# Performance work log

Measured on AMD Instinct MI355X. Metric: run time of the kernel, lower is better.

The kernel has to match this reference:

```python
import jax, jax.numpy as jnp
import numpy as np
from jax import lax

EPS = 1e-9
DN = ('NCHW', 'OIHW', 'NCHW')


def _conv2d_valid(x, w):
    return lax.conv_general_dilated(x, w, window_strides=(1, 1), padding='VALID',
                                    dimension_numbers=DN)


def setup_inputs() -> dict:
    key = jax.random.key(0)
    kx, ky = jax.random.split(key)
    x = jax.random.normal(kx, (32, 64, 96, 96), dtype=jnp.float32)
    y = jax.random.normal(ky, (32, 64, 13, 13), dtype=jnp.float32)  # (K prototypes, C, kh, kw)
    return {'x': x, 'y': y}


def reference(x, y):
    # Per-prototype L2 normalization of y over (C, kh, kw)
    y_norm = jnp.clip(jnp.sqrt(jnp.sum(y * y, axis=(1, 2, 3), keepdims=True)), EPS)
    normed_y = y / y_norm
    # Sliding-window L2 norm of x. The torch code convolves x^2 with ones of
    # shape (K, C, kh, kw) producing K identical channels; we compute one
    # channel and broadcast (same math, less work).
    ones_k = jnp.ones((1,) + y.shape[1:], dtype=x.dtype)
    x_norm = jnp.clip(jnp.sqrt(_conv2d_valid(x * x, ones_k)), EPS)  # (B,1,H',W')
    diss = _conv2d_valid(x, normed_y) / x_norm  # (B,K,H',W')
    return jax.nn.relu(diss)
```

## Files before the change

kernel.cpp:

```cpp
#include <hip/hip_runtime.h>
#include <hip/hip_bf16.h>

#define B_   32
#define C_   64
#define H_   96
#define W_   96
#define K_   32
#define R_   13
#define HO_  84
#define WO_  84
#define HW_  (H_*W_)
#define OHW_ (HO_*WO_)
#define CRR_ (C_*R_*R_)
#define RR_  (R_*R_)

#define TILE_ 16
#define PW_   28
#define TLV_  24
#define PH_   36
#define NPIX2_ (PH_*PW_)
#define NEL2_  (2*NPIX2_)
#define HB2_   (NPIX2_*16)
#define BUF2_  (2*HB2_)
#define NPIX_ (PW_*PW_)
#define REGB_ (NPIX_*16)
#define LDS_FB (2*REGB_)

#define XBF_BYTES  ((size_t)B_*4*HW_*32)
#define UG_BYTES   ((size_t)RR_*4096)
#define S_BYTES    ((size_t)B_*HW_*4)
#define INV_BYTES  ((size_t)B_*OHW_*4)
#define WS_NEED    (XBF_BYTES + UG_BYTES + S_BYTES + INV_BYTES)

typedef unsigned int u32;
typedef unsigned short u16;
typedef __attribute__((ext_vector_type(16))) float f32x16;
typedef __attribute__((ext_vector_type(4))) u32 u32x4;

static __device__ __forceinline__ u16 f2bf(float v){
    __hip_bfloat16 h = __float2bfloat16(v);
    return *reinterpret_cast<u16*>(&h);
}

#define MFMA(acc, a, b) asm("v_mfma_f32_32x32x16_bf16 %0, %1, %2, %0" \
                            : "+v"(acc) : "v"(a), "v"(b))

static __device__ __forceinline__ void gload_lds16(const void* g, void* l){
    __builtin_amdgcn_global_load_lds(
        (const __attribute__((address_space(1))) unsigned char*)g,
        (__attribute__((address_space(3))) unsigned char*)l, 16, 0, 0);
}

static __device__ void prep_y_block(const float* __restrict__ y,
                                    unsigned char* __restrict__ u_g,
                                    int k, int tid, float* red){
    const float* yk = y + (size_t)k * CRR_;
    float ss = 0.f;
    for (int idx = tid; idx < CRR_; idx += 256){ float v = yk[idx]; ss += v*v; }
    for (int off = 32; off; off >>= 1) ss += __shfl_down(ss, off);
    if ((tid & 63) == 0) red[tid >> 6] = ss;
    __syncthreads();
    float inv = 1.f / fmaxf(sqrtf(red[0]+red[1]+red[2]+red[3]), 1e-9f);

    int c = tid & 63, grp = tid >> 6;
    int inoff = (k << 5) | ((c & 15) << 1);
    for (int base = 0; base < RR_; base += 4){
        int ij = base + grp;
        if (ij < RR_){
            int i = ij / R_, jx = ij % R_;
            float v = yk[c*RR_ + ij] * inv;
            size_t slice = ((size_t)(c >> 4) * RR_ + jx*R_ + i) << 10;
            *(u16*)(u_g + slice + inoff) = f2bf(v);
        }
    }
}

__global__ void k_prep_y(const float* __restrict__ y, unsigned char* __restrict__ u_g){
    __shared__ float red[4];
    prep_y_block(y, u_g, blockIdx.x, threadIdx.x, red);
}

__global__ void k_prep(const float* __restrict__ x, const float* __restrict__ y,
                       float* __restrict__ s, unsigned char* __restrict__ xbf,
                       unsigned char* __restrict__ u_g){
    __shared__ float red[4];
    int bb = blockIdx.x;
    if (bb < K_){ prep_y_block(y, u_g, bb, threadIdx.x, red); return; }
    int idx = (bb - K_)*256 + threadIdx.x;
    int b = idx / HW_, r = idx % HW_;
    const float* xb = x + (size_t)b * C_ * HW_ + r;
    float acc = 0.f;
    #pragma unroll
    for (int q = 0; q < 4; ++q){
        int c0 = q*16;
        float a0 = xb[(size_t)(c0+0)*HW_],  a1 = xb[(size_t)(c0+1)*HW_];
        float a2 = xb[(size_t)(c0+2)*HW_],  a3 = xb[(size_t)(c0+3)*HW_];
        float a4 = xb[(size_t)(c0+4)*HW_],  a5 = xb[(size_t)(c0+5)*HW_];
        float a6 = xb[(size_t)(c0+6)*HW_],  a7 = xb[(size_t)(c0+7)*HW_];
        float a8 = xb[(size_t)(c0+8)*HW_],  a9 = xb[(size_t)(c0+9)*HW_];
        float aa = xb[(size_t)(c0+10)*HW_], ab = xb[(size_t)(c0+11)*HW_];
        float ac = xb[(size_t)(c0+12)*HW_], ad = xb[(size_t)(c0+13)*HW_];
        float ae = xb[(size_t)(c0+14)*HW_], af = xb[(size_t)(c0+15)*HW_];
        acc += a0*a0+a1*a1+a2*a2+a3*a3+a4*a4+a5*a5+a6*a6+a7*a7
             + a8*a8+a9*a9+aa*aa+ab*ab+ac*ac+ad*ad+ae*ae+af*af;
        u32x4 q0 = { f2bf(a0)|((u32)f2bf(a1)<<16), f2bf(a2)|((u32)f2bf(a3)<<16),
                     f2bf(a4)|((u32)f2bf(a5)<<16), f2bf(a6)|((u32)f2bf(a7)<<16) };
        u32x4 q1 = { f2bf(a8)|((u32)f2bf(a9)<<16), f2bf(aa)|((u32)f2bf(ab)<<16),
                     f2bf(ac)|((u32)f2bf(ad)<<16), f2bf(ae)|((u32)f2bf(af)<<16) };
        unsigned char* ob = xbf + ((size_t)(b*4 + q)*HW_ + r)*32;
        *(u32x4*)(ob)      = q0;
        *(u32x4*)(ob + 16) = q1;
    }
    s[idx] = acc;
}

__global__ void k_sq(const float* __restrict__ x, float* __restrict__ s){
    int idx = blockIdx.x*256 + threadIdx.x;
    int b = idx / HW_, r = idx % HW_;
    const float* xb = x + (size_t)b * C_ * HW_;
    float acc = 0.f;
    #pragma unroll
    for (int c = 0; c < C_; ++c){ float v = xb[(size_t)c*HW_ + r]; acc += v*v; }
    s[idx] = acc;
}

__global__ void k_inv(const float* __restrict__ s, float* __restrict__ inv_xn){
    int idx = blockIdx.x*256 + threadIdx.x;
    int b = idx / OHW_, r = idx % OHW_;
    int oh = r / WO_, ow = r % WO_;
    const float* sb = s + (size_t)b*HW_ + oh*W_ + ow;
    float acc = 0.f;
    for (int i = 0; i < R_; ++i){
        #pragma unroll
        for (int j = 0; j < R_; ++j) acc += sb[i*W_ + j];
    }
    inv_xn[idx] = 1.f / fmaxf(sqrtf(acc), 1e-9f);
}

__launch_bounds__(256, 3)
__global__ void k_main(const unsigned char* __restrict__ xbf,
                       const unsigned char* __restrict__ u_g,
                       const float* __restrict__ inv_xn, float* __restrict__ out){
    extern __shared__ unsigned char lds[];

    int bb0 = blockIdx.x;
    int bb  = (bb0 & 7) * 96 + (bb0 >> 3);
    int b  = bb / 24;
    int tt = bb % 24;
    int oy = (tt / 6) * TLV_;
    int ox = (tt % 6) * TILE_;

    int tid  = threadIdx.x;
    int lane = tid & 63;
    int wv   = tid >> 6;
    int ks   = lane >> 5;
    int rb   = (lane >> 4) & 1;
    int cx   = lane & 15;
    int kpr  = lane & 31;

    const unsigned char* xq = xbf + (size_t)b*4*HW_*32;
    int aoff = (kpr << 5) + (ks << 4);
    int pb   = (6*wv + rb) * PW_ + cx;

    int goff[8], loff[8];
    #pragma unroll
    for (int j = 0; j < 8; ++j){
        int cb = wv + 4*j;
        int cs = cb*64; if (cs > NEL2_-64) cs = NEL2_-64;
        int e = cs + lane;
        int h = (e >= NPIX2_);
        int p = e - (h ? NPIX2_ : 0);
        int py = p / PW_, px = p % PW_;
        int gy = oy + py; if (gy > H_-1) gy = H_-1;
        int gx = ox + px; if (gx > W_-1) gx = W_-1;
        goff[j] = ((gy*W_ + gx) << 5) + h*16;
        loff[j] = cs << 4;
    }

#define STAGE(q) {                                                           \
        const unsigned char* src = xq + (size_t)(q)*HW_*32;                  \
        _Pragma("unroll")                                                    \
        for (int j = 0; j < 8; ++j)                                          \
            gload_lds16(src + goff[j], lds + loff[j]);                       \
    }

    f32x16 acc0 = {}, acc1 = {}, acc2 = {};
    STAGE(0);
    __syncthreads();

    for (int pass = 0; pass < 4; ++pass){
        const unsigned char* xh = lds + ks*HB2_;
        const unsigned char* ug = u_g + ((size_t)pass*RR_ << 10);

        u32x4 A0 = *(const u32x4*)(ug              + aoff);
        u32x4 A1 = *(const u32x4*)(ug + (1 << 10)  + aoff);
        u32x4 A2 = *(const u32x4*)(ug + (2 << 10)  + aoff);
        u32x4 A3 = *(const u32x4*)(ug + (3 << 10)  + aoff);

        const unsigned char* col0 = xh + pb*16;
        u32x4 w0 = *(const u32x4*)(col0);
        u32x4 w1 = *(const u32x4*)(col0 +   PW_*16);
        u32x4 w2 = *(const u32x4*)(col0 + 2*PW_*16);
        u32x4 w3 = *(const u32x4*)(col0 + 3*PW_*16);
        u32x4 w4 = *(const u32x4*)(col0 + 4*PW_*16);
        u32x4 w5 = *(const u32x4*)(col0 + 5*PW_*16);

        int t = 0;
        for (int jx = 0; jx < R_; ++jx){
            const unsigned char* col  = xh + (pb + jx)*16;
            const unsigned char* ncol = col + 16;
            u32x4 e0, e1, e2, e3, e4, e5;
            #pragma unroll
            for (int i = 0; i < R_; ++i, ++t){
                int tn = t + 4; if (tn > RR_-1) tn = RR_-1;
                u32x4 An = *(const u32x4*)(ug + ((size_t)tn << 10) + aoff);
                u32x4 wn = w5;
                if (i < 11) wn = *(const u32x4*)(col + (i+6)*PW_*16);
                if (i == 7)  e0 = *(const u32x4*)(ncol);
                if (i == 8)  e1 = *(const u32x4*)(ncol +   PW_*16);
                if (i == 9)  e2 = *(const u32x4*)(ncol + 2*PW_*16);
                if (i == 10) e3 = *(const u32x4*)(ncol + 3*PW_*16);
                if (i == 11) e4 = *(const u32x4*)(ncol + 4*PW_*16);
                if (i == 12) e5 = *(const u32x4*)(ncol + 5*PW_*16);
                __builtin_amdgcn_s_setprio(1);
                MFMA(acc0, A0, w0);
                MFMA(acc1, A0, w2);
                MFMA(acc2, A0, w4);
                __builtin_amdgcn_s_setprio(0);
                A0 = A1; A1 = A2; A2 = A3; A3 = An;
                w0 = w1; w1 = w2; w2 = w3; w3 = w4; w4 = w5; w5 = wn;
            }
            w0 = e0; w1 = e1; w2 = e2; w3 = e3; w4 = e4; w5 = e5;
        }

        if (pass < 3){
            __syncthreads();
            STAGE(pass+1);
            __syncthreads();
        }
    }

    int ow = ox + cx;
#define EPI(ACC, F) {                                                        \
        int oh = oy + 6*wv + rb + 2*(F);                                     \
        bool valid = (oh < HO_) && (ow < WO_);                               \
        float inv = 0.f;                                                     \
        if (valid) inv = inv_xn[(size_t)b*OHW_ + oh*WO_ + ow];               \
        float* ob = out + (size_t)b*K_*OHW_ + oh*WO_ + ow;                   \
        _Pragma("unroll")                                                    \
        for (int r = 0; r < 16; ++r){                                        \
            int kp = (r & 3) + 8*(r >> 2) + 4*ks;                            \
            if (valid) ob[(size_t)kp*OHW_] = fmaxf(ACC[r], 0.f) * inv;       \
        }                                                                    \
    }
    EPI(acc0, 0); EPI(acc1, 1); EPI(acc2, 2);
#undef EPI
}

__launch_bounds__(256, 4)
__global__ void k_main_fb(const float* __restrict__ x, const unsigned char* __restrict__ u_g,
                          const float* __restrict__ inv_xn, float* __restrict__ out){
    extern __shared__ unsigned char lds[];
    int bb = blockIdx.x;
    int b  = bb / 36;
    int tt = bb % 36;
    int oy = (tt / 6) * TILE_;
    int ox = (tt % 6) * TILE_;
    int tid  = threadIdx.x;
    int lane = tid & 63;
    int wv   = tid >> 6;
    int ks   = lane >> 5;
    int rb   = (lane >> 4) & 1;
    int cx   = lane & 15;
    int kpr  = lane & 31;
    const float* xb = x + (size_t)b * C_ * HW_;
    int aoff = (kpr << 5) + (ks << 4);
    int pb   = (4*wv + rb) * PW_ + cx;
    f32x16 acc0 = {}, acc1 = {};
    for (int pass = 0; pass < 4; ++pass){
        if (pass) __syncthreads();
        int cbase = pass << 4;
        for (int p = tid; p < NPIX_; p += 256){
            int py = p / PW_, px = p % PW_;
            int gy = oy + py; if (gy > H_-1) gy = H_-1;
            int gx = ox + px; if (gx > W_-1) gx = W_-1;
            const float* src = xb + (size_t)cbase*HW_ + gy*W_ + gx;
            u32 w0 = f2bf(src[0*HW_])  | ((u32)f2bf(src[1*HW_])  << 16);
            u32 w1 = f2bf(src[2*HW_])  | ((u32)f2bf(src[3*HW_])  << 16);
            u32 w2 = f2bf(src[4*HW_])  | ((u32)f2bf(src[5*HW_])  << 16);
            u32 w3 = f2bf(src[6*HW_])  | ((u32)f2bf(src[7*HW_])  << 16);
            u32x4 q0 = {w0, w1, w2, w3};
            u32 v0 = f2bf(src[8*HW_])  | ((u32)f2bf(src[9*HW_])  << 16);
            u32 v1 = f2bf(src[10*HW_]) | ((u32)f2bf(src[11*HW_]) << 16);
            u32 v2 = f2bf(src[12*HW_]) | ((u32)f2bf(src[13*HW_]) << 16);
            u32 v3 = f2bf(src[14*HW_]) | ((u32)f2bf(src[15*HW_]) << 16);
            u32x4 q1 = {v0, v1, v2, v3};
            *(u32x4*)(lds +         p*16) = q0;
            *(u32x4*)(lds + REGB_ + p*16) = q1;
        }
        __syncthreads();
        const unsigned char* xh = lds + ks*REGB_;
        const unsigned char* ug = u_g + ((size_t)pass*RR_ << 10);
        u32x4 A0 = *(const u32x4*)(ug              + aoff);
        u32x4 A1 = *(const u32x4*)(ug + (1 << 10)  + aoff);
        u32x4 A2 = *(const u32x4*)(ug + (2 << 10)  + aoff);
        u32x4 A3 = *(const u32x4*)(ug + (3 << 10)  + aoff);
        int t = 0;
        for (int jx = 0; jx < R_; ++jx){
            const unsigned char* col = xh + (pb + jx)*16;
            u32x4 d0 = *(const u32x4*)(col);
            u32x4 d1 = *(const u32x4*)(col +   PW_*16);
            u32x4 d2 = *(const u32x4*)(col + 2*PW_*16);
            u32x4 d3 = *(const u32x4*)(col + 3*PW_*16);
            u32x4 d4 = *(const u32x4*)(col + 4*PW_*16);
            #pragma unroll
            for (int i = 0; i < R_; ++i, ++t){
                int tn = t + 4; if (tn > RR_-1) tn = RR_-1;
                u32x4 An = *(const u32x4*)(ug + ((size_t)tn << 10) + aoff);
                u32x4 dn = d4;
                if (i < 10) dn = *(const u32x4*)(col + (i+5)*PW_*16);
                MFMA(acc0, A0, d0);
                MFMA(acc1, A0, d2);
                A0 = A1; A1 = A2; A2 = A3; A3 = An;
                d0 = d1; d1 = d2; d2 = d3; d3 = d4; d4 = dn;
            }
        }
    }
    int ow = ox + cx;
#define EPI(ACC, F) {                                                        \
        int oh = oy + 4*wv + rb + 2*(F);                                     \
        bool valid = (oh < HO_) && (ow < WO_);                               \
        float inv = 0.f;                                                     \
        if (valid) inv = inv_xn[(size_t)b*OHW_ + oh*WO_ + ow];               \
        float* ob = out + (size_t)b*K_*OHW_ + oh*WO_ + ow;                   \
        _Pragma("unroll")                                                    \
        for (int r = 0; r < 16; ++r){                                        \
            int kp = (r & 3) + 8*(r >> 2) + 4*ks;                            \
            if (valid) ob[(size_t)kp*OHW_] = fmaxf(ACC[r], 0.f) * inv;       \
        }                                                                    \
    }
    EPI(acc0, 0); EPI(acc1, 1);
#undef EPI
}

extern "C" void kernel_launch(void* const* d_in, const int* in_sizes, int n_in,
                              void* d_out, int out_size, void* d_ws, size_t ws_size,
                              hipStream_t stream) {
    const float* x = (const float*)d_in[0];
    const float* y = (const float*)d_in[1];
    float* out = (float*)d_out;
    unsigned char* ws = (unsigned char*)d_ws;

    if (ws_size >= WS_NEED){
        unsigned char* xbf   = ws;
        unsigned char* u_g   = ws + XBF_BYTES;
        float*         s     = (float*)(ws + XBF_BYTES + UG_BYTES);
        float*         invxn = (float*)(ws + XBF_BYTES + UG_BYTES + S_BYTES);

        k_prep<<<K_ + (B_*HW_)/256, 256, 0, stream>>>(x, y, s, xbf, u_g);
        k_inv<<<(B_*OHW_)/256, 256, 0, stream>>>(s, invxn);
        k_main<<<B_*24, 256, BUF2_, stream>>>(xbf, u_g, invxn, out);
    } else {
        unsigned char* u_g   = ws;
        float*         s     = (float*)(ws + UG_BYTES);
        float*         invxn = (float*)(ws + UG_BYTES + S_BYTES);

        k_prep_y<<<K_, 256, 0, stream>>>(y, u_g);
        k_sq<<<(B_*HW_)/256, 256, 0, stream>>>(x, s);
        k_inv<<<(B_*OHW_)/256, 256, 0, stream>>>(s, invxn);
        k_main_fb<<<B_*36, 256, LDS_FB, stream>>>(x, u_g, invxn, out);
    }
}
```

Measured before the change: 198.7 us.

## Retile main conv kernel to 32-wide by 12-tall output tiles

Changes the output tile from 16x24 to 32x12. Each wave now covers 32 columns by 3 rows with one MFMA column per row, so the sliding register window shrinks from six rows to three. The grid becomes 21 tiles per batch instead of 24, and the tiles divide 84 exactly, which removes vertical padding waste and the row-validity checks. The LDS halo grows to 44x24, giving more staged bytes per output and nine load chunks instead of eight. Fewer register rows could ease pressure, but the per-pixel halo overhead shifts.

```diff
diff --git a/kernel.cpp b/kernel.cpp
--- a/kernel.cpp
+++ b/kernel.cpp
@@ -16,12 +16,14 @@
 
 #define TILE_ 16
 #define PW_   28
-#define TLV_  24
-#define PH_   36
-#define NPIX2_ (PH_*PW_)
-#define NEL2_  (2*NPIX2_)
-#define HB2_   (NPIX2_*16)
-#define BUF2_  (2*HB2_)
+#define TLH_  32
+#define TLV3_ 12
+#define PWW_  44
+#define PHH_  24
+#define NPIX3_ (PHH_*PWW_)
+#define NEL3_  (2*NPIX3_)
+#define HB3_   (NPIX3_*16)
+#define BUF3_  (2*HB3_)
 #define NPIX_ (PW_*PW_)
 #define REGB_ (NPIX_*16)
 #define LDS_FB (2*REGB_)
@@ -144,34 +146,33 @@
     extern __shared__ unsigned char lds[];
 
     int bb0 = blockIdx.x;
-    int bb  = (bb0 & 7) * 96 + (bb0 >> 3);
-    int b  = bb / 24;
-    int tt = bb % 24;
-    int oy = (tt / 6) * TLV_;
-    int ox = (tt % 6) * TILE_;
+    int bb  = (bb0 & 7) * 84 + (bb0 >> 3);
+    int b  = bb / 21;
+    int tt = bb % 21;
+    int oy = (tt / 3) * TLV3_;
+    int ox = (tt % 3) * TLH_;
 
     int tid  = threadIdx.x;
     int lane = tid & 63;
     int wv   = tid >> 6;
     int ks   = lane >> 5;
-    int rb   = (lane >> 4) & 1;
-    int cx   = lane & 15;
+    int nn   = lane & 31;
     int kpr  = lane & 31;
 
     const unsigned char* xq = xbf + (size_t)b*4*HW_*32;
     int aoff = (kpr << 5) + (ks << 4);
-    int pb   = (6*wv + rb) * PW_ + cx;
-
-    int goff[8], loff[8];
+    int pb3  = (3*wv)*PWW_ + nn;
+
+    int goff[9], loff[9];
     #pragma unroll
-    for (int j = 0; j < 8; ++j){
+    for (int j = 0; j < 9; ++j){
         int cb = wv + 4*j;
-        int cs = cb*64; if (cs > NEL2_-64) cs = NEL2_-64;
+        int cs = cb*64; if (cs > NEL3_-64) cs = NEL3_-64;
         int e = cs + lane;
-        int h = (e >= NPIX2_);
-        int p = e - (h ? NPIX2_ : 0);
-        int py = p / PW_, px = p % PW_;
-        int gy = oy + py; if (gy > H_-1) gy = H_-1;
+        int h = (e >= NPIX3_);
+        int p = e - (h ? NPIX3_ : 0);
+        int py = p / PWW_, px = p % PWW_;
+        int gy = oy + py;
         int gx = ox + px; if (gx > W_-1) gx = W_-1;
         goff[j] = ((gy*W_ + gx) << 5) + h*16;
         loff[j] = cs << 4;
@@ -180,7 +181,7 @@
 #define STAGE(q) {                                                           \
         const unsigned char* src = xq + (size_t)(q)*HW_*32;                  \
         _Pragma("unroll")                                                    \
-        for (int j = 0; j < 8; ++j)                                          \
+        for (int j = 0; j < 9; ++j)                                          \
             gload_lds16(src + goff[j], lds + loff[j]);                       \
     }
 
@@ -189,7 +190,7 @@
     __syncthreads();
 
     for (int pass = 0; pass < 4; ++pass){
-        const unsigned char* xh = lds + ks*HB2_;
+        const unsigned char* xh = lds + ks*HB3_;
         const unsigned char* ug = u_g + ((size_t)pass*RR_ << 10);
 
         u32x4 A0 = *(const u32x4*)(ug              + aoff);
@@ -197,40 +198,34 @@
         u32x4 A2 = *(const u32x4*)(ug + (2 << 10)  + aoff);
         u32x4 A3 = *(const u32x4*)(ug + (3 << 10)  + aoff);
 
-        const unsigned char* col0 = xh + pb*16;
+        const unsigned char* col0 = xh + pb3*16;
         u32x4 w0 = *(const u32x4*)(col0);
-        u32x4 w1 = *(const u32x4*)(col0 +   PW_*16);
-        u32x4 w2 = *(const u32x4*)(col0 + 2*PW_*16);
-        u32x4 w3 = *(const u32x4*)(col0 + 3*PW_*16);
-        u32x4 w4 = *(const u32x4*)(col0 + 4*PW_*16);
-        u32x4 w5 = *(const u32x4*)(col0 + 5*PW_*16);
+        u32x4 w1 = *(const u32x4*)(col0 +   PWW_*16);
+        u32x4 w2 = *(const u32x4*)(col0 + 2*PWW_*16);
 
         int t = 0;
         for (int jx = 0; jx < R_; ++jx){
-            const unsigned char* col  = xh + (pb + jx)*16;
+            const unsigned char* col  = xh + (pb3 + jx)*16;
             const unsigned char* ncol = col + 16;
-            u32x4 e0, e1, e2, e3, e4, e5;
+            u32x4 e0, e1, e2;
             #pragma unroll
             for (int i = 0; i < R_; ++i, ++t){
                 int tn = t + 4; if (tn > RR_-1) tn = RR_-1;
                 u32x4 An = *(const u32x4*)(ug + ((size_t)tn << 10) + aoff);
-                u32x4 wn = w5;
-                if (i < 11) wn = *(const u32x4*)(col + (i+6)*PW_*16);
-                if (i == 7)  e0 = *(const u32x4*)(ncol);
-                if (i == 8)  e1 = *(const u32x4*)(ncol +   PW_*16);
-                if (i == 9)  e2 = *(const u32x4*)(ncol + 2*PW_*16);
-                if (i == 10) e3 = *(const u32x4*)(ncol + 3*PW_*16);
-                if (i == 11) e4 = *(const u32x4*)(ncol + 4*PW_*16);
-                if (i == 12) e5 = *(const u32x4*)(ncol + 5*PW_*16);
+                u32x4 wn = w2;
+                if (i < 12) wn = *(const u32x4*)(col + (i+3)*PWW_*16);
+                if (i == 9)  e0 = *(const u32x4*)(ncol);
+                if (i == 10) e1 = *(const u32x4*)(ncol +   PWW_*16);
+                if (i == 11) e2 = *(const u32x4*)(ncol + 2*PWW_*16);
                 __builtin_amdgcn_s_setprio(1);
                 MFMA(acc0, A0, w0);
-                MFMA(acc1, A0, w2);
-                MFMA(acc2, A0, w4);
+                MFMA(acc1, A0, w1);
+                MFMA(acc2, A0, w2);
                 __builtin_amdgcn_s_setprio(0);
                 A0 = A1; A1 = A2; A2 = A3; A3 = An;
-                w0 = w1; w1 = w2; w2 = w3; w3 = w4; w4 = w5; w5 = wn;
+                w0 = w1; w1 = w2; w2 = wn;
             }
-            w0 = e0; w1 = e1; w2 = e2; w3 = e3; w4 = e4; w5 = e5;
+            w0 = e0; w1 = e1; w2 = e2;
         }
 
         if (pass < 3){
@@ -240,10 +235,10 @@
         }
     }
 
-    int ow = ox + cx;
+    int ow = ox + nn;
+    bool valid = (ow < WO_);
 #define EPI(ACC, F) {                                                        \
-        int oh = oy + 6*wv + rb + 2*(F);                                     \
-        bool valid = (oh < HO_) && (ow < WO_);                               \
+        int oh = oy + 3*wv + (F);                                            \
         float inv = 0.f;                                                     \
         if (valid) inv = inv_xn[(size_t)b*OHW_ + oh*WO_ + ow];               \
         float* ob = out + (size_t)b*K_*OHW_ + oh*WO_ + ow;                   \
@@ -359,7 +354,7 @@
 
         k_prep<<<K_ + (B_*HW_)/256, 256, 0, stream>>>(x, y, s, xbf, u_g);
         k_inv<<<(B_*OHW_)/256, 256, 0, stream>>>(s, invxn);
-        k_main<<<B_*24, 256, BUF2_, stream>>>(xbf, u_g, invxn, out);
+        k_main<<<B_*21, 256, BUF3_, stream>>>(xbf, u_g, invxn, out);
     } else {
         unsigned char* u_g   = ws;
         float*         s     = (float*)(ws + UG_BYTES);
```

Result: faster. 187.2 us (-5.8%).
